# Optimization experiments

Hardware: AMD Instinct MI355X
Metric: run time of the kernel (lower is better)

The kernel has to match this reference:

```python
import jax, jax.numpy as jnp
import numpy as np

B, T, D = 2, 2048, 2048
H, HD = 16, 128
ROPE_BASE = 10000.0
EPS = 1e-6


def setup_inputs() -> dict:
    key = jax.random.key(0)
    ks = jax.random.split(key, 5)
    s = 1.0 / np.sqrt(D)
    return {
        "x": jax.random.normal(ks[0], (B, T, D), dtype=jnp.float32),
        "Wq": jax.random.normal(ks[1], (H * HD, D), dtype=jnp.float32) * s,
        "Wk": jax.random.normal(ks[2], (H * HD, D), dtype=jnp.float32) * s,
        "Wv": jax.random.normal(ks[3], (H * HD, D), dtype=jnp.float32) * s,
        "Wo": jax.random.normal(ks[4], (D, H * HD), dtype=jnp.float32) * s,
        "q_norm_w": jnp.ones((HD,), dtype=jnp.float32),
        "k_norm_w": jnp.ones((HD,), dtype=jnp.float32),
    }


def _rms_norm(x, w):
    # RMSNorm over last dim, no centering (LLaMA/Qwen style)
    norm = jnp.sqrt(jnp.mean(jnp.square(x), axis=-1, keepdims=True) + EPS)
    return x / norm * w


def _rope_interleaved(x):
    # x: (B, T, H, HD); GPT-NeoX interleaved style, sequential positions
    dim = HD // 2
    freqs = jnp.exp(-jnp.arange(0, dim, dtype=jnp.float32) * jnp.log(ROPE_BASE) / dim)
    angles = jnp.arange(T, dtype=jnp.float32)[:, None] * freqs[None, :]  # (T, dim)
    cos = jnp.cos(angles)[None, :, None, :]  # (1, T, 1, dim)
    sin = jnp.sin(angles)[None, :, None, :]
    x_even = x[..., ::2]
    x_odd = x[..., 1::2]
    r_even = x_even * cos - x_odd * sin
    r_odd = x_even * sin + x_odd * cos
    return jnp.stack([r_even, r_odd], axis=-1).reshape(x.shape)


def reference(x, Wq, Wk, Wv, Wo, q_norm_w, k_norm_w):
    # QKV projections (weights stored [out, in], per llm_linear einsum)
    q = jnp.einsum("btd,od->bto", x, Wq).reshape(B, T, H, HD)
    k = jnp.einsum("btd,od->bto", x, Wk).reshape(B, T, H, HD)
    v = jnp.einsum("btd,od->bto", x, Wv).reshape(B, T, H, HD)
    # per-head QK RMSNorm
    q = _rms_norm(q, q_norm_w)
    k = _rms_norm(k, k_norm_w)
    # rotary embeddings
    q = _rope_interleaved(q)
    k = _rope_interleaved(k)
    # causal scaled dot-product attention
    scale = 1.0 / jnp.sqrt(jnp.asarray(HD, dtype=x.dtype))
    scores = jnp.einsum("bthd,bshd->bhts", q, k) * scale  # (B, H, T, T)
    causal = jnp.tril(jnp.ones((T, T), dtype=bool))
    scores = jnp.where(causal[None, None, :, :], scores, jnp.asarray(-1e30, dtype=scores.dtype))
    probs = jax.nn.softmax(scores, axis=-1)
    ctx = jnp.einsum("bhts,bshd->bthd", probs, v).reshape(B, T, H * HD)
    # output projection
    return jnp.einsum("bto,do->btd", ctx, Wo)
```

## Files before the change

kernel.cpp:

```cpp
#include <hip/hip_runtime.h>
#include <cstdint>
#include <cstddef>

#define B_ 2
#define T_ 2048
#define D_ 2048
#define H_ 16
#define HD_ 128
#define EPS_ 1e-6f
#define QSCALE_ 0.08838834764831845f
#define KVSTRIDE_ (H_ * HD_)

typedef unsigned short u16;
typedef short s16x8 __attribute__((ext_vector_type(8)));
typedef float f32x4 __attribute__((ext_vector_type(4)));

__device__ __forceinline__ float bf2f(u16 h) {
  union { unsigned int u; float f; } v;
  v.u = ((unsigned int)h) << 16;
  return v.f;
}
__device__ __forceinline__ u16 f2bf(float f) {
  union { float f; unsigned int u; } v;
  v.f = f;
  unsigned int r = v.u + 0x7FFFu + ((v.u >> 16) & 1u);
  return (u16)(r >> 16);
}

__device__ __forceinline__ void gload16(const void* g, void* l) {
  __builtin_amdgcn_global_load_lds(
      (const __attribute__((address_space(1))) unsigned int*)g,
      (__attribute__((address_space(3))) unsigned int*)l, 16, 0, 0);
}

__global__ void cvt_f32_bf16(const float* __restrict__ in, u16* __restrict__ out, int n4) {
  int i = blockIdx.x * blockDim.x + threadIdx.x;
  if (i < n4) {
    float4 v = ((const float4*)in)[i];
    ((ushort4*)out)[i] = make_ushort4(f2bf(v.x), f2bf(v.y), f2bf(v.z), f2bf(v.w));
  }
}

template <int OUT_BF16>
__global__ __launch_bounds__(256, 2) void gemm_btn(const u16* __restrict__ A,
                                                   const u16* __restrict__ Bm,
                                                   void* __restrict__ Cout,
                                                   int M, int N, int K) {
  __shared__ u16 As[2 * 128 * 32];
  __shared__ u16 Bs[2 * 128 * 32];
  const int tid = threadIdx.x;
  const int w = tid >> 6, lane = tid & 63, quad = lane >> 4, c = lane & 15;
  const int wm = w & 1, wn = w >> 1;
  const int m0 = blockIdx.y * 128, n0 = blockIdx.x * 128;

  f32x4 acc[4][4];
#pragma unroll
  for (int i = 0; i < 4; ++i)
#pragma unroll
    for (int j = 0; j < 4; ++j) acc[i][j] = (f32x4){0.f, 0.f, 0.f, 0.f};

  for (int k0 = 0; k0 < K; k0 += 64) {
    __syncthreads();
#pragma unroll
    for (int i = 0; i < 4; ++i) {
      int chunk = (w * 4 + i) * 64 + lane;
      int kc = chunk >> 9;
      int within = chunk & 511;
      int row = within >> 2, cc = within & 3;
      gload16(A + (size_t)(m0 + row) * K + k0 + kc * 32 + cc * 8, (void*)(As + chunk * 8));
      gload16(Bm + (size_t)(n0 + row) * K + k0 + kc * 32 + cc * 8, (void*)(Bs + chunk * 8));
    }
    __syncthreads();
#pragma unroll
    for (int kc = 0; kc < 2; ++kc) {
      s16x8 af[4], bf[4];
#pragma unroll
      for (int mi = 0; mi < 4; ++mi)
        af[mi] = *(const s16x8*)(As + kc * 4096 + (wm * 64 + mi * 16 + c) * 32 + quad * 8);
#pragma unroll
      for (int ni = 0; ni < 4; ++ni)
        bf[ni] = *(const s16x8*)(Bs + kc * 4096 + (wn * 64 + ni * 16 + c) * 32 + quad * 8);
#pragma unroll
      for (int mi = 0; mi < 4; ++mi)
#pragma unroll
        for (int ni = 0; ni < 4; ++ni)
          acc[mi][ni] = __builtin_amdgcn_mfma_f32_16x16x32_bf16(af[mi], bf[ni], acc[mi][ni], 0, 0, 0);
    }
  }

#pragma unroll
  for (int mi = 0; mi < 4; ++mi)
#pragma unroll
    for (int ni = 0; ni < 4; ++ni)
#pragma unroll
      for (int r = 0; r < 4; ++r) {
        int row = m0 + wm * 64 + mi * 16 + quad * 4 + r;
        int col = n0 + wn * 64 + ni * 16 + c;
        float v = acc[mi][ni][r];
        if (OUT_BF16)
          ((u16*)Cout)[(size_t)row * N + col] = f2bf(v);
        else
          ((float*)Cout)[(size_t)row * N + col] = v;
      }
}

__global__ void rmsnorm_rope(u16* __restrict__ x, const float* __restrict__ nw, float outscale) {
  const int tid = threadIdx.x;
  const int w = tid >> 6, lane = tid & 63;
  const int vec = blockIdx.x * 4 + w;
  const int t = (vec >> 4) & (T_ - 1);
  u16* base = x + (size_t)vec * HD_;
  unsigned int pk = *(const unsigned int*)(base + lane * 2);
  float e = bf2f((u16)(pk & 0xFFFFu));
  float o = bf2f((u16)(pk >> 16));
  float ss = e * e + o * o;
#pragma unroll
  for (int off = 1; off < 64; off <<= 1) ss += __shfl_xor(ss, off, 64);
  float rn = rsqrtf(ss * (1.0f / HD_) + EPS_);
  float we = nw[lane * 2], wo = nw[lane * 2 + 1];
  e = e * rn * we;
  o = o * rn * wo;
  float freq = expf(-(float)lane * (9.210340371976184f / 64.0f));
  float ang = (float)t * freq;
  float sn, cs;
  sincosf(ang, &sn, &cs);
  float re = (e * cs - o * sn) * outscale;
  float ro = (e * sn + o * cs) * outscale;
  *(unsigned int*)(base + lane * 2) = ((unsigned int)f2bf(ro) << 16) | (unsigned int)f2bf(re);
}

__global__ __launch_bounds__(256, 2) void attn_fwd(const u16* __restrict__ Q,
                                                   const u16* __restrict__ Kg,
                                                   const u16* __restrict__ Vt,
                                                   u16* __restrict__ O) {
  __shared__ u16 Ks[64 * 128];
  __shared__ u16 Vts[128 * 64];
  __shared__ u16 Ps[64 * 64];
  const int tid = threadIdx.x;
  const int w = tid >> 6, lane = tid & 63, quad = lane >> 4, c = lane & 15;
  const int c7 = (c & 7) * 8;
  const int bid = blockIdx.x;
  const int qt = 31 - (bid >> 5);
  const int h = bid & 15;
  const int b = (bid >> 4) & 1;
  const int q0 = qt * 64;

  s16x8 qf[4];
  const u16* qbase = Q + ((size_t)(b * T_ + q0 + w * 16 + c) * H_ + h) * HD_;
#pragma unroll
  for (int kk = 0; kk < 4; ++kk) qf[kk] = *(const s16x8*)(qbase + kk * 32 + quad * 8);

  f32x4 of[8];
#pragma unroll
  for (int i = 0; i < 8; ++i) of[i] = (f32x4){0.f, 0.f, 0.f, 0.f};
  float m_i[4] = {-1e30f, -1e30f, -1e30f, -1e30f};
  float l_i[4] = {0.f, 0.f, 0.f, 0.f};

  const u16* kbase = Kg + ((size_t)b * T_ * H_ + h) * HD_;
  const u16* vtbase = Vt + (size_t)(h * HD_) * (B_ * T_) + (size_t)b * T_;

  for (int j = 0; j <= qt; ++j) {
    __syncthreads();
    const u16* krow = kbase + (size_t)(j * 64) * KVSTRIDE_;
    const u16* vrow = vtbase + j * 64;
#pragma unroll
    for (int i = 0; i < 4; ++i) {
      int chunk = i * 256 + tid;
      int krowi = chunk >> 4, kslot = (chunk & 15) ^ (krowi & 7);
      gload16(krow + (size_t)krowi * KVSTRIDE_ + kslot * 8, (void*)(Ks + chunk * 8));
      int vrowi = chunk >> 3, vslot = (chunk & 7) ^ (vrowi & 7);
      gload16(vrow + (size_t)vrowi * (B_ * T_) + vslot * 8, (void*)(Vts + chunk * 8));
    }
    __syncthreads();

    f32x4 sf[4];
#pragma unroll
    for (int ni = 0; ni < 4; ++ni) {
      f32x4 a = (f32x4){0.f, 0.f, 0.f, 0.f};
#pragma unroll
      for (int kk = 0; kk < 4; ++kk) {
        s16x8 bfr = *(const s16x8*)(&Ks[(ni * 16 + c) * 128 + ((kk * 32 + quad * 8) ^ c7)]);
        a = __builtin_amdgcn_mfma_f32_16x16x32_bf16(qf[kk], bfr, a, 0, 0, 0);
      }
      sf[ni] = a;
    }
    if (j == qt) {
#pragma unroll
      for (int ni = 0; ni < 4; ++ni)
#pragma unroll
        for (int r = 0; r < 4; ++r) {
          int rowg = w * 16 + quad * 4 + r;
          int colg = ni * 16 + c;
          if (colg > rowg) sf[ni][r] = -1e30f;
        }
    }
    float mc[4];
#pragma unroll
    for (int r = 0; r < 4; ++r)
      mc[r] = fmaxf(fmaxf(sf[0][r], sf[1][r]), fmaxf(sf[2][r], sf[3][r]));
#pragma unroll
    for (int off = 1; off < 16; off <<= 1)
#pragma unroll
      for (int r = 0; r < 4; ++r) mc[r] = fmaxf(mc[r], __shfl_xor(mc[r], off, 64));
#pragma unroll
    for (int r = 0; r < 4; ++r) {
      float mnew = fmaxf(m_i[r], mc[r]);
      float alpha = __expf(m_i[r] - mnew);
      m_i[r] = mnew;
      l_i[r] *= alpha;
#pragma unroll
      for (int ot = 0; ot < 8; ++ot) of[ot][r] *= alpha;
    }
    float rs[4] = {0.f, 0.f, 0.f, 0.f};
#pragma unroll
    for (int ni = 0; ni < 4; ++ni)
#pragma unroll
      for (int r = 0; r < 4; ++r) {
        float p = __expf(sf[ni][r] - m_i[r]);
        sf[ni][r] = p;
        rs[r] += p;
      }
#pragma unroll
    for (int off = 1; off < 16; off <<= 1)
#pragma unroll
      for (int r = 0; r < 4; ++r) rs[r] += __shfl_xor(rs[r], off, 64);
#pragma unroll
    for (int r = 0; r < 4; ++r) l_i[r] += rs[r];
#pragma unroll
    for (int ni = 0; ni < 4; ++ni)
#pragma unroll
      for (int r = 0; r < 4; ++r) {
        int row = w * 16 + quad * 4 + r;
        Ps[row * 64 + ((ni * 16 + c) ^ ((row & 7) * 8))] = f2bf(sf[ni][r]);
      }
    s16x8 pa[2];
    pa[0] = *(const s16x8*)(&Ps[(w * 16 + c) * 64 + ((quad * 8) ^ c7)]);
    pa[1] = *(const s16x8*)(&Ps[(w * 16 + c) * 64 + ((32 + quad * 8) ^ c7)]);
#pragma unroll
    for (int ot = 0; ot < 8; ++ot) {
#pragma unroll
      for (int kk = 0; kk < 2; ++kk) {
        s16x8 vfr = *(const s16x8*)(&Vts[(ot * 16 + c) * 64 + ((kk * 32 + quad * 8) ^ c7)]);
        of[ot] = __builtin_amdgcn_mfma_f32_16x16x32_bf16(pa[kk], vfr, of[ot], 0, 0, 0);
      }
    }
  }

  float inv[4];
#pragma unroll
  for (int r = 0; r < 4; ++r) inv[r] = 1.0f / l_i[r];
  u16* obase = O + ((size_t)(b * T_ + q0) * H_ + h) * HD_;
#pragma unroll
  for (int ot = 0; ot < 8; ++ot)
#pragma unroll
    for (int r = 0; r < 4; ++r)
      obase[(size_t)(w * 16 + quad * 4 + r) * KVSTRIDE_ + ot * 16 + c] = f2bf(of[ot][r] * inv[r]);
}

extern "C" void kernel_launch(void* const* d_in, const int* in_sizes, int n_in,
                              void* d_out, int out_size, void* d_ws, size_t ws_size,
                              hipStream_t stream) {
  const float* x = (const float*)d_in[0];
  const float* Wq = (const float*)d_in[1];
  const float* Wk = (const float*)d_in[2];
  const float* Wv = (const float*)d_in[3];
  const float* Wo = (const float*)d_in[4];
  const float* qw = (const float*)d_in[5];
  const float* kw = (const float*)d_in[6];
  float* out = (float*)d_out;

  const size_t xE = (size_t)B_ * T_ * D_;
  const size_t wE = (size_t)D_ * H_ * HD_;
  const size_t need = xE * 2 * 5 + wE * 2 * 4;
  if (ws_size < need) return;

  char* ws = (char*)d_ws;
  u16* xb = (u16*)ws;   ws += xE * 2;
  u16* wqb = (u16*)ws;  ws += wE * 2;
  u16* wkb = (u16*)ws;  ws += wE * 2;
  u16* wvb = (u16*)ws;  ws += wE * 2;
  u16* wob = (u16*)ws;  ws += wE * 2;
  u16* qb = (u16*)ws;   ws += xE * 2;
  u16* kb = (u16*)ws;   ws += xE * 2;
  u16* vtb = (u16*)ws;  ws += xE * 2;
  u16* ctxb = (u16*)ws; ws += xE * 2;

  cvt_f32_bf16<<<xE / 1024, 256, 0, stream>>>(x, xb, (int)(xE / 4));
  cvt_f32_bf16<<<wE / 1024, 256, 0, stream>>>(Wq, wqb, (int)(wE / 4));
  cvt_f32_bf16<<<wE / 1024, 256, 0, stream>>>(Wk, wkb, (int)(wE / 4));
  cvt_f32_bf16<<<wE / 1024, 256, 0, stream>>>(Wv, wvb, (int)(wE / 4));
  cvt_f32_bf16<<<wE / 1024, 256, 0, stream>>>(Wo, wob, (int)(wE / 4));

  dim3 gg(16, 32);
  gemm_btn<1><<<gg, 256, 0, stream>>>(xb, wqb, qb, 4096, 2048, 2048);
  gemm_btn<1><<<gg, 256, 0, stream>>>(xb, wkb, kb, 4096, 2048, 2048);
  dim3 ggv(32, 16);
  gemm_btn<1><<<ggv, 256, 0, stream>>>(wvb, xb, vtb, 2048, 4096, 2048);

  rmsnorm_rope<<<16384, 256, 0, stream>>>(qb, qw, QSCALE_);
  rmsnorm_rope<<<16384, 256, 0, stream>>>(kb, kw, 1.0f);

  attn_fwd<<<B_ * H_ * (T_ / 64), 256, 0, stream>>>(qb, kb, vtb, ctxb);

  gemm_btn<0><<<gg, 256, 0, stream>>>(ctxb, wob, out, 4096, 2048, 2048);
}
```

Before: 422.0 us.

## Double-buffer K/V tiles in attention and defer row-sum reduction to epilogue

Splits the K and V shared-memory tiles into two buffers and issues the global loads for tile j+1 before computing on tile j. This aims to hide global-load latency behind the MFMA and softmax work, and it cuts the loop to one barrier per iteration instead of two. It also drops the per-iteration cross-lane shuffle reduction of the softmax row sum. Each lane keeps a partial sum that is rescaled by the row-uniform alpha, and the lanes reduce once after the loop. The cost is twice the K/V LDS footprint, about 72KB per block, which could limit occupancy with two blocks per CU.

```diff
diff --git a/kernel.cpp b/kernel.cpp
--- a/kernel.cpp
+++ b/kernel.cpp
@@ -133,8 +133,8 @@
                                                    const u16* __restrict__ Kg,
                                                    const u16* __restrict__ Vt,
                                                    u16* __restrict__ O) {
-  __shared__ u16 Ks[64 * 128];
-  __shared__ u16 Vts[128 * 64];
+  __shared__ u16 Ks[2][64 * 128];
+  __shared__ u16 Vts[2][128 * 64];
   __shared__ u16 Ps[64 * 64];
   const int tid = threadIdx.x;
   const int w = tid >> 6, lane = tid & 63, quad = lane >> 4, c = lane & 15;
@@ -154,24 +154,30 @@
 #pragma unroll
   for (int i = 0; i < 8; ++i) of[i] = (f32x4){0.f, 0.f, 0.f, 0.f};
   float m_i[4] = {-1e30f, -1e30f, -1e30f, -1e30f};
-  float l_i[4] = {0.f, 0.f, 0.f, 0.f};
+  float lp[4] = {0.f, 0.f, 0.f, 0.f};
 
   const u16* kbase = Kg + ((size_t)b * T_ * H_ + h) * HD_;
   const u16* vtbase = Vt + (size_t)(h * HD_) * (B_ * T_) + (size_t)b * T_;
 
-  for (int j = 0; j <= qt; ++j) {
-    __syncthreads();
+  auto STAGE = [&](int j, int buf) {
     const u16* krow = kbase + (size_t)(j * 64) * KVSTRIDE_;
     const u16* vrow = vtbase + j * 64;
 #pragma unroll
     for (int i = 0; i < 4; ++i) {
       int chunk = i * 256 + tid;
       int krowi = chunk >> 4, kslot = (chunk & 15) ^ (krowi & 7);
-      gload16(krow + (size_t)krowi * KVSTRIDE_ + kslot * 8, (void*)(Ks + chunk * 8));
+      gload16(krow + (size_t)krowi * KVSTRIDE_ + kslot * 8, (void*)(&Ks[buf][0] + chunk * 8));
       int vrowi = chunk >> 3, vslot = (chunk & 7) ^ (vrowi & 7);
-      gload16(vrow + (size_t)vrowi * (B_ * T_) + vslot * 8, (void*)(Vts + chunk * 8));
-    }
-    __syncthreads();
+      gload16(vrow + (size_t)vrowi * (B_ * T_) + vslot * 8, (void*)(&Vts[buf][0] + chunk * 8));
+    }
+  };
+
+  STAGE(0, 0);
+  __syncthreads();
+  int cur = 0;
+
+  for (int j = 0; j <= qt; ++j) {
+    if (j < qt) STAGE(j + 1, cur ^ 1);
 
     f32x4 sf[4];
 #pragma unroll
@@ -179,7 +185,7 @@
       f32x4 a = (f32x4){0.f, 0.f, 0.f, 0.f};
 #pragma unroll
       for (int kk = 0; kk < 4; ++kk) {
-        s16x8 bfr = *(const s16x8*)(&Ks[(ni * 16 + c) * 128 + ((kk * 32 + quad * 8) ^ c7)]);
+        s16x8 bfr = *(const s16x8*)(&Ks[cur][(ni * 16 + c) * 128 + ((kk * 32 + quad * 8) ^ c7)]);
         a = __builtin_amdgcn_mfma_f32_16x16x32_bf16(qf[kk], bfr, a, 0, 0, 0);
       }
       sf[ni] = a;
@@ -207,25 +213,18 @@
       float mnew = fmaxf(m_i[r], mc[r]);
       float alpha = __expf(m_i[r] - mnew);
       m_i[r] = mnew;
-      l_i[r] *= alpha;
+      lp[r] *= alpha;
 #pragma unroll
       for (int ot = 0; ot < 8; ++ot) of[ot][r] *= alpha;
     }
-    float rs[4] = {0.f, 0.f, 0.f, 0.f};
 #pragma unroll
     for (int ni = 0; ni < 4; ++ni)
 #pragma unroll
       for (int r = 0; r < 4; ++r) {
         float p = __expf(sf[ni][r] - m_i[r]);
         sf[ni][r] = p;
-        rs[r] += p;
-      }
-#pragma unroll
-    for (int off = 1; off < 16; off <<= 1)
-#pragma unroll
-      for (int r = 0; r < 4; ++r) rs[r] += __shfl_xor(rs[r], off, 64);
-#pragma unroll
-    for (int r = 0; r < 4; ++r) l_i[r] += rs[r];
+        lp[r] += p;
+      }
 #pragma unroll
     for (int ni = 0; ni < 4; ++ni)
 #pragma unroll
@@ -240,15 +239,22 @@
     for (int ot = 0; ot < 8; ++ot) {
 #pragma unroll
       for (int kk = 0; kk < 2; ++kk) {
-        s16x8 vfr = *(const s16x8*)(&Vts[(ot * 16 + c) * 64 + ((kk * 32 + quad * 8) ^ c7)]);
+        s16x8 vfr = *(const s16x8*)(&Vts[cur][(ot * 16 + c) * 64 + ((kk * 32 + quad * 8) ^ c7)]);
         of[ot] = __builtin_amdgcn_mfma_f32_16x16x32_bf16(pa[kk], vfr, of[ot], 0, 0, 0);
       }
     }
+
+    __syncthreads();
+    cur ^= 1;
   }
 
+#pragma unroll
+  for (int off = 1; off < 16; off <<= 1)
+#pragma unroll
+    for (int r = 0; r < 4; ++r) lp[r] += __shfl_xor(lp[r], off, 64);
   float inv[4];
 #pragma unroll
-  for (int r = 0; r < 4; ++r) inv[r] = 1.0f / l_i[r];
+  for (int r = 0; r < 4; ++r) inv[r] = 1.0f / lp[r];
   u16* obase = O + ((size_t)(b * T_ + q0) * H_ + h) * HD_;
 #pragma unroll
   for (int ot = 0; ot < 8; ++ot)
```

After: 411.8 us. 1.02x faster.
